# Optimization experiments

Hardware: AMD Instinct MI355X
Metric: run time of the kernel (lower is better)

## Reference

```python
import jax, jax.numpy as jnp
import numpy as np

HEAD_NUM = 16
QKV_DIM = 32
EMB = 512
SQRT_EMB = 22.627416997969522  # sqrt(512)
LOGIT_CLIP = 10.0
BATCH, POMO, PROBLEM = 32, 256, 1024


def setup_inputs() -> dict:
    key = jax.random.key(0)
    ks = jax.random.split(key, 8)
    s = 0.02
    return {
        "encoded_nodes": jax.random.normal(ks[0], (BATCH, PROBLEM, EMB), jnp.float32),
        "encoded_q1": jax.random.normal(ks[1], (BATCH, POMO, EMB), jnp.float32),
        "encoded_last_node": jax.random.normal(ks[2], (BATCH, POMO, EMB), jnp.float32),
        "ninf_mask": jnp.zeros((BATCH, POMO, PROBLEM), jnp.float32),
        # weights stored [in, out] so y = x @ W (equiv. to torch Linear with W.T)
        "Wq_first": jax.random.normal(ks[3], (EMB, HEAD_NUM * QKV_DIM), jnp.float32) * s,
        "Wq_last": jax.random.normal(ks[4], (EMB, HEAD_NUM * QKV_DIM), jnp.float32) * s,
        "Wk": jax.random.normal(ks[5], (EMB, HEAD_NUM * QKV_DIM), jnp.float32) * s,
        "Wv": jax.random.normal(ks[6], (EMB, HEAD_NUM * QKV_DIM), jnp.float32) * s,
        "W_combine": jax.random.normal(ks[7], (HEAD_NUM * QKV_DIM, EMB), jnp.float32) * s,
        "b_combine": jnp.zeros((EMB,), jnp.float32),
    }


def _heads(x):
    # [b, n, h*d] -> [b, h, n, d]
    b, n, _ = x.shape
    return x.reshape(b, n, HEAD_NUM, QKV_DIM).transpose(0, 2, 1, 3)


def reference(encoded_nodes, encoded_q1, encoded_last_node, ninf_mask,
              Wq_first, Wq_last, Wk, Wv, W_combine, b_combine):
    # set_kv
    k = _heads(encoded_nodes @ Wk)                     # [b,h,problem,d]
    v = _heads(encoded_nodes @ Wv)                     # [b,h,problem,d]
    single_head_key = encoded_nodes.transpose(0, 2, 1) # [b,emb,problem]
    # set_q1
    q_first = _heads(encoded_q1 @ Wq_first)            # [b,h,pomo,d]
    # forward
    q_last = _heads(encoded_last_node @ Wq_last)       # [b,h,pomo,d]
    q = q_first + q_last

    scale = 1.0 / jnp.sqrt(jnp.asarray(QKV_DIM, q.dtype))
    score = jnp.einsum("bhnd,bhmd->bhnm", q, k) * scale  # [b,h,pomo,problem]
    score = score + ninf_mask[:, None, :, :]
    weights = jax.nn.softmax(score, axis=-1)
    out = jnp.einsum("bhnm,bhmd->bhnd", weights, v)      # [b,h,pomo,d]
    out_concat = out.transpose(0, 2, 1, 3).reshape(q.shape[0], q.shape[2], HEAD_NUM * QKV_DIM)
    mh_out = out_concat @ W_combine + b_combine          # [b,pomo,emb]

    score2 = jnp.einsum("bne,bem->bnm", mh_out, single_head_key) / SQRT_EMB
    score2 = LOGIT_CLIP * jnp.tanh(score2) + ninf_mask
    probs = jax.nn.softmax(score2, axis=2)               # [b,pomo,problem]
    return probs
```

## Files before the change

### kernel.cpp

```cpp
#include <hip/hip_runtime.h>
#include <math.h>

typedef unsigned short u16;
typedef __attribute__((ext_vector_type(8))) short bf16x8;
typedef __attribute__((ext_vector_type(4))) float f32x4;
typedef __attribute__((ext_vector_type(4))) int i32x4;
typedef __attribute__((ext_vector_type(4))) short s16x4;
typedef __attribute__((ext_vector_type(4))) unsigned short u16x4;

#define MFMA16(a,b,c) __builtin_amdgcn_mfma_f32_16x16x32_bf16((a),(b),(c),0,0,0)

__device__ __forceinline__ u16 f2bf(float x){
  unsigned int u = __float_as_uint(x);
  u += 0x7fffu + ((u >> 16) & 1u);
  return (u16)(u >> 16);
}
__device__ __forceinline__ float bf2f(u16 x){
  return __uint_as_float(((unsigned)x) << 16);
}
__device__ __forceinline__ void gload16(const void* g, void* l){
  __builtin_amdgcn_global_load_lds((const __attribute__((address_space(1))) void*)g,
                                   (__attribute__((address_space(3))) void*)l, 16, 0, 0);
}

__global__ __launch_bounds__(256) void prep(
    const float* __restrict__ nodes, const float* __restrict__ q1, const float* __restrict__ lastn,
    const float* __restrict__ mask,
    const float* __restrict__ Wqf, const float* __restrict__ Wql, const float* __restrict__ Wk,
    const float* __restrict__ Wv, const float* __restrict__ Wc,
    u16* __restrict__ qlbP,
    u16* __restrict__ WtKV, u16* __restrict__ WtQ2, u16* __restrict__ WtCP,
    u16* __restrict__ nodesP, u16* __restrict__ maskP)
{
  const int tid = blockIdx.x * 256 + threadIdx.x;

  #pragma unroll
  for (int it = 0; it < 2; ++it) {
    int id = tid + it*1048576;
    int ln = id & 15, q = (id >> 4) & 3, kc = (id >> 6) & 15, cb = (id >> 10) & 63, b = id >> 16;
    const float* s = nodes + ((b*1024 + cb*16 + ln)*512 + kc*32 + q*8);
    float4 v0 = *(const float4*)s, v1 = *(const float4*)(s+4);
    u16 o[8];
    o[0]=f2bf(v0.x); o[1]=f2bf(v0.y); o[2]=f2bf(v0.z); o[3]=f2bf(v0.w);
    o[4]=f2bf(v1.x); o[5]=f2bf(v1.y); o[6]=f2bf(v1.z); o[7]=f2bf(v1.w);
    *(i32x4*)&nodesP[id*8] = *(i32x4*)&o[0];
  }

  {
    int ln = tid & 15, q = (tid >> 4) & 3, kc = (tid >> 6) & 31, mblk = tid >> 11;
    int m = mblk*16 + ln, k = kc*32 + q*8;
    const float* s = (k < 512) ? (q1 + m*512 + k) : (lastn + m*512 + (k - 512));
    float4 v0 = *(const float4*)s, v1 = *(const float4*)(s+4);
    u16 o[8];
    o[0]=f2bf(v0.x); o[1]=f2bf(v0.y); o[2]=f2bf(v0.z); o[3]=f2bf(v0.w);
    o[4]=f2bf(v1.x); o[5]=f2bf(v1.y); o[6]=f2bf(v1.z); o[7]=f2bf(v1.w);
    *(i32x4*)&qlbP[tid*8] = *(i32x4*)&o[0];
  }

  if (tid < 262144) {
    int n = tid >> 9, k = tid & 511;
    WtQ2[n*1024 + k]       = f2bf(Wqf[k*512 + n]);
    WtQ2[n*1024 + 512 + k] = f2bf(Wql[k*512 + n]);
  }
  if (tid < 524288) {
    int n = tid >> 9, k = tid & 511;
    WtKV[tid] = f2bf(n < 512 ? Wk[k*512 + n] : Wv[k*512 + (n-512)]);
  }
  if (tid < 32768) {
    int ln = tid & 15, q = (tid >> 4) & 3, kc = (tid >> 6) & 15, cb = tid >> 10;
    u16 o[8];
    #pragma unroll
    for (int e=0;e<8;e++) o[e] = f2bf(Wc[(kc*32 + q*8 + e)*512 + cb*16 + ln]);
    *(i32x4*)&WtCP[tid*8] = *(i32x4*)&o[0];
  }
  if (tid < 524288) {
    int brt = tid >> 10, c = tid & 1023;
    const float* mp = mask + (brt*16)*1024 + c;
    u16 vals[16];
    #pragma unroll
    for (int p=0;p<16;p++) vals[p] = f2bf(mp[p*1024]);
    u16* dst = maskP + (brt*64 + (c >> 4))*256 + (c & 15)*4;
    #pragma unroll
    for (int q4=0;q4<4;q4++) {
      u16x4 v; v[0]=vals[q4*4]; v[1]=vals[q4*4+1]; v[2]=vals[q4*4+2]; v[3]=vals[q4*4+3];
      *(u16x4*)&dst[q4*64] = v;
    }
  }
}

__global__ __launch_bounds__(512, 2) void kvq(
    const u16* __restrict__ Akv, const u16* __restrict__ Bkv,
    const u16* __restrict__ Aq,  const u16* __restrict__ Bq,
    u16* __restrict__ Kout, u16* __restrict__ Vout, u16* __restrict__ Qout)
{
  __shared__ u16 smem[24576];
  const int t = threadIdx.x, w = t >> 6, l = t & 63, q = l >> 4, ln = l & 15;
  const int wr = w >> 2, wc = w & 3;
  const int wm = wr * 64, wn = wc * 64;

  const bool isq = blockIdx.x < 128;
  int mb, nb, ksteps, kstr, KC;
  const u16 *Ab, *Bb;
  if (isq) {
    const int bid = blockIdx.x;
    mb = bid >> 1; nb = bid & 1;
    ksteps = 32; kstr = 1024; KC = 32; Ab = Aq; Bb = Bq;
  } else {
    const int bid = blockIdx.x - 128;
    mb = (bid >> 5)*8 + (bid & 7);
    nb = (bid >> 3) & 3;
    ksteps = 16; kstr = 512; KC = 16; Ab = Akv; Bb = Bkv;
  }
  const int m0 = mb*128, n0 = nb*256;

  f32x4 acc[4][4];
  #pragma unroll
  for (int i=0;i<4;i++)
    #pragma unroll
    for (int j=0;j<4;j++)
      #pragma unroll
      for (int r=0;r<4;r++) acc[i][j][r] = 0.f;

  const u16* ApL  = Ab + (((m0 >> 4) + (t >> 6))*KC*64 + (t & 63))*8;
  const u16* Baddr = Bb + (n0 + (t & 255))*kstr + (t >> 8)*8;

  #define STAGE(kc_, b_) { \
    u16* s = smem + (b_)*12288; \
    gload16(ApL + (kc_)*512,       &s[t*8]); \
    gload16(Baddr + (kc_)*32,      &s[4096 + t*8]); \
    gload16(Baddr + 16 + (kc_)*32, &s[4096 + (t+512)*8]); }

  STAGE(0, 0);
  for (int kc = 0; kc < ksteps; kc++) {
    __syncthreads();
    if (kc + 1 < ksteps) STAGE(kc+1, (kc+1)&1);
    const u16* sa = smem + (kc&1)*12288;
    const u16* sb = sa + 4096;
    const int acb = wm >> 4;
    bf16x8 af[4], bfr[4];
    #pragma unroll
    for (int i=0;i<4;i++) af[i]  = *(bf16x8*)&sa[((acb + i)*4 + q)*128 + ln*8];
    #pragma unroll
    for (int j=0;j<4;j++) bfr[j] = *(bf16x8*)&sb[(q*256 + wn + j*16 + ln)*8];
    #pragma unroll
    for (int i=0;i<4;i++)
      #pragma unroll
      for (int j=0;j<4;j++)
        acc[i][j] = MFMA16(af[i], bfr[j], acc[i][j]);
  }
  #undef STAGE

  const float scale = isq ? 0.17677669529663687f : 1.0f;
  const int bb_ = mb >> 3, mloc = (mb & 7)*128;
  const int bbq = mb >> 1, pm0 = (mb & 1)*128;
  for (int h = 0; h < 4; ++h) {
    __syncthreads();
    if (wc == h) {
      #pragma unroll
      for (int i=0;i<4;i++)
        #pragma unroll
        for (int j=0;j<4;j++) {
          s16x4 o;
          #pragma unroll
          for (int r=0;r<4;r++) o[r] = (short)f2bf(acc[i][j][r]*scale);
          *(s16x4*)&smem[(j*16 + ln)*140 + wm + i*16 + q*4] = o;
        }
    }
    __syncthreads();
    #pragma unroll
    for (int hc=0; hc<2; ++hc) {
      if (isq) {
        const int head = nb*8 + h*2 + hc;
        const int m_ = t >> 2, d0 = (t & 3)*8;
        u16 v[8];
        #pragma unroll
        for (int dd=0;dd<8;dd++) v[dd] = smem[(hc*32 + d0 + dd)*140 + m_];
        *(i32x4*)&Qout[((bbq*16 + head)*256 + pm0 + m_)*32 + d0] = *(i32x4*)&v[0];
      } else if (nb < 2) {
        const int head = nb*8 + h*2 + hc;
        const int m_ = t >> 2, d0 = (t & 3)*8;
        u16 v[8];
        #pragma unroll
        for (int dd=0;dd<8;dd++) v[dd] = smem[(hc*32 + d0 + dd)*140 + m_];
        *(i32x4*)&Kout[((bb_*16 + head)*1024 + mloc + m_)*32 + d0] = *(i32x4*)&v[0];
      } else {
        const int vh = (nb-2)*8 + h*2 + hc;
        const int d = t >> 4, mo = (t & 15)*8;
        *(i32x4*)&Vout[((bb_*16 + vh)*32 + d)*1024 + mloc + mo]
            = *(i32x4*)&smem[(hc*32 + d)*140 + mo];
      }
    }
  }
}

__global__ __launch_bounds__(256) void attn(const u16* __restrict__ Qg, const u16* __restrict__ Kg,
                                            const u16* __restrict__ Vtg, const u16* __restrict__ maskP,
                                            u16* __restrict__ Og)
{
  const int bid = blockIdx.x;
  const int bh = (bid & 7)*64 + (bid >> 3);
  const int h = bh & 15, bb = bh >> 4;
  const int t = threadIdx.x, w = t >> 6, l = t & 63, q = l >> 4, ln = l & 15;
  __shared__ u16 Qs[8192];
  __shared__ u16 Ks[4096];
  __shared__ u16 Vs[4096];
  __shared__ u16 Ps[2560];
  u16* Pw = &Ps[w*640];
  const int qbase = (bb*16 + h)*256*32;
  #pragma unroll
  for (int c=0;c<4;c++)
    gload16(&Qg[qbase + t*32 + c*8], &Qs[(c*256 + t)*8]);
  const int kbase = (bb*16 + h)*1024*32;
  const int vbase = (bb*16 + h)*32*1024;
  float rs[4][4];
  f32x4 oacc[4][2];
  #pragma unroll
  for (int rg=0;rg<4;rg++) {
    #pragma unroll
    for (int r=0;r<4;r++) rs[rg][r] = 0.f;
    #pragma unroll
    for (int dt=0;dt<2;dt++)
      #pragma unroll
      for (int r=0;r<4;r++) oacc[rg][dt][r] = 0.f;
  }
  __syncthreads();
  bf16x8 aq[4];
  #pragma unroll
  for (int rg=0;rg<4;rg++) aq[rg] = *(bf16x8*)&Qs[(q*256 + w*64 + rg*16 + ln)*8];
  const u16* mbase = maskP + (bb*16 + w*4)*16384 + q*64 + ln*4;
  u16x4 mqA[8], mqB[8];

  #define RG_BODY(rg, MQC, MQN) { \
    if ((rg) < 3) { \
      _Pragma("unroll") \
      for (int j2=0;j2<8;j2++) \
        MQN[j2] = *(const u16x4*)&mbase[((rg)+1)*16384 + (mc*8 + j2)*256]; \
    } \
    _Pragma("unroll") \
    for (int ch=0; ch<4; ch++) { \
      bf16x8 bk0 = *(bf16x8*)&Ks[(q*128 + (ch*2+0)*16 + ln)*8]; \
      bf16x8 bk1 = *(bf16x8*)&Ks[(q*128 + (ch*2+1)*16 + ln)*8]; \
      f32x4 zz = {0.f,0.f,0.f,0.f}; \
      f32x4 s0 = MFMA16(aq[rg], bk0, zz); \
      f32x4 s1 = MFMA16(aq[rg], bk1, zz); \
      _Pragma("unroll") \
      for (int r=0;r<4;r++) { \
        float e0 = __expf(s0[r] + bf2f(MQC[ch*2+0][r])); \
        float e1 = __expf(s1[r] + bf2f(MQC[ch*2+1][r])); \
        rs[rg][r] += e0 + e1; \
        Pw[(q*4+r)*40 + ln]      = f2bf(e0); \
        Pw[(q*4+r)*40 + 16 + ln] = f2bf(e1); \
      } \
      bf16x8 ap  = *(bf16x8*)&Pw[ln*40 + q*8]; \
      bf16x8 bv0 = *(bf16x8*)&Vs[((ch*4+q)*32 + ln)*8]; \
      bf16x8 bv1 = *(bf16x8*)&Vs[((ch*4+q)*32 + 16 + ln)*8]; \
      oacc[rg][0] = MFMA16(ap, bv0, oacc[rg][0]); \
      oacc[rg][1] = MFMA16(ap, bv1, oacc[rg][1]); \
    } }

  for (int mc = 0; mc < 8; mc++) {
    __syncthreads();
    gload16(&Kg[kbase + (mc*128 + (t & 127))*32 + (t >> 7)*8],       &Ks[t*8]);
    gload16(&Kg[kbase + (mc*128 + (t & 127))*32 + ((t >> 7)+2)*8],   &Ks[(t+256)*8]);
    gload16(&Vtg[vbase + (t & 31)*1024 + mc*128 + (t >> 5)*8],       &Vs[t*8]);
    gload16(&Vtg[vbase + (t & 31)*1024 + mc*128 + ((t >> 5)+8)*8],   &Vs[(t+256)*8]);
    #pragma unroll
    for (int j2=0;j2<8;j2++)
      mqA[j2] = *(const u16x4*)&mbase[(mc*8 + j2)*256];
    __syncthreads();
    RG_BODY(0, mqA, mqB)
    RG_BODY(1, mqB, mqA)
    RG_BODY(2, mqA, mqB)
    RG_BODY(3, mqB, mqA)
  }
  #undef RG_BODY

  #pragma unroll
  for (int rg=0;rg<4;rg++) {
    #pragma unroll
    for (int r=0;r<4;r++) {
      float v = rs[rg][r];
      v += __shfl_xor(v,1); v += __shfl_xor(v,2); v += __shfl_xor(v,4); v += __shfl_xor(v,8);
      rs[rg][r] = __builtin_amdgcn_rcpf(v);
    }
    const int orow = bb*256 + w*64 + rg*16 + q*4;
    #pragma unroll
    for (int dt=0;dt<2;dt++)
      #pragma unroll
      for (int r=0;r<4;r++)
        Og[(orow + r)*512 + h*32 + dt*16 + ln] = f2bf(oacc[rg][dt][r]*rs[rg][r]);
  }
}

__global__ __launch_bounds__(1024) void cmbfin(const u16* __restrict__ oc, const u16* __restrict__ WtCP,
                                               const float* __restrict__ bias,
                                               const u16* __restrict__ nodesP, const u16* __restrict__ maskP,
                                               float* __restrict__ out)
{
  const int bid = blockIdx.x;
  const int bb = bid & 31, rg = bid >> 5;
  const int t = threadIdx.x, w = t >> 6, l = t & 63, q = l >> 4, ln = l & 15;
  __shared__ u16 As[16384];
  __shared__ u16 Ms[16384];
  __shared__ float rsL[16][32];
  const int abase = (bb*256 + rg*32)*512;
  #pragma unroll
  for (int c=0;c<2;c++) {
    int chunk = t + 1024*c;
    gload16(&oc[abase + (chunk & 31)*512 + (chunk >> 5)*8], &As[chunk*8]);
  }
  __syncthreads();
  f32x4 acc1[2][2];
  #pragma unroll
  for (int i=0;i<2;i++)
    #pragma unroll
    for (int ct=0;ct<2;ct++)
      #pragma unroll
      for (int r=0;r<4;r++) acc1[i][ct][r] = 0.f;
  for (int kc=0;kc<16;kc++) {
    bf16x8 af[2];
    #pragma unroll
    for (int i=0;i<2;i++) af[i] = *(bf16x8*)&As[((kc*4 + q)*32 + i*16 + ln)*8];
    #pragma unroll
    for (int ct=0;ct<2;ct++) {
      bf16x8 bfr = *(const bf16x8*)&WtCP[(((w*2 + ct)*16 + kc)*4 + q)*128 + ln*8];
      #pragma unroll
      for (int i=0;i<2;i++) acc1[i][ct] = MFMA16(af[i], bfr, acc1[i][ct]);
    }
  }
  #pragma unroll
  for (int ct=0;ct<2;ct++) {
    int gn = w*32 + ct*16 + ln;
    float bv = bias[gn];
    #pragma unroll
    for (int i=0;i<2;i++)
      #pragma unroll
      for (int r=0;r<4;r++)
        Ms[(gn >> 3)*256 + (i*16 + q*4 + r)*8 + (gn & 7)] = f2bf(acc1[i][ct][r] + bv);
  }
  __syncthreads();
  float rloc[2][4] = {{0.f,0.f,0.f,0.f},{0.f,0.f,0.f,0.f}};
  const int nbase = bb*524288;
  f32x4 acc[2][4];
  #pragma unroll
  for (int i=0;i<2;i++)
    #pragma unroll
    for (int ct=0;ct<4;ct++)
      #pragma unroll
      for (int r=0;r<4;r++) acc[i][ct][r] = 0.f;
  for (int kc=0;kc<16;kc++) {
    bf16x8 af[2];
    #pragma unroll
    for (int i=0;i<2;i++) af[i] = *(bf16x8*)&Ms[((kc*4 + q)*32 + i*16 + ln)*8];
    #pragma unroll
    for (int ct=0;ct<4;ct++) {
      bf16x8 bfr = *(const bf16x8*)&nodesP[nbase + (((w*4 + ct)*16 + kc)*4 + q)*128 + ln*8];
      #pragma unroll
      for (int i=0;i<2;i++) acc[i][ct] = MFMA16(af[i], bfr, acc[i][ct]);
    }
  }
  const float c2 = 0.08838834764831843f;
  const int prow_base = bb*256 + rg*32;
  #pragma unroll
  for (int i=0;i<2;i++) {
    #pragma unroll
    for (int ct=0;ct<4;ct++) {
      u16x4 mv = *(const u16x4*)&maskP[((bb*16 + rg*2 + i)*64 + w*4 + ct)*256 + q*64 + ln*4];
      #pragma unroll
      for (int r=0;r<4;r++) {
        float x = acc[i][ct][r] * c2;
        x = fminf(fmaxf(x, -30.f), 30.f);
        float e2 = __expf(x);
        float lg = 10.f*(e2 - 1.f)*__builtin_amdgcn_rcpf(e2 + 1.f) + bf2f(mv[r]);
        float e = __expf(lg);
        rloc[i][r] += e;
        acc[i][ct][r] = e;
      }
    }
  }
  #pragma unroll
  for (int i=0;i<2;i++)
    #pragma unroll
    for (int r=0;r<4;r++) {
      float v = rloc[i][r];
      v += __shfl_xor(v,1); v += __shfl_xor(v,2); v += __shfl_xor(v,4); v += __shfl_xor(v,8);
      rloc[i][r] = v;
    }
  if (ln == 0) {
    #pragma unroll
    for (int i=0;i<2;i++)
      #pragma unroll
      for (int r=0;r<4;r++) rsL[w][i*16 + q*4 + r] = rloc[i][r];
  }
  __syncthreads();
  float inv[2][4];
  #pragma unroll
  for (int i=0;i<2;i++)
    #pragma unroll
    for (int r=0;r<4;r++) {
      float tot = 0.f;
      #pragma unroll
      for (int ww=0;ww<16;ww++) tot += rsL[ww][i*16 + q*4 + r];
      inv[i][r] = __builtin_amdgcn_rcpf(tot);
    }
  #pragma unroll
  for (int i=0;i<2;i++)
    #pragma unroll
    for (int ct=0;ct<4;ct++) {
      int col0 = w*64 + ct*16 + ln;
      #pragma unroll
      for (int r=0;r<4;r++)
        out[(prow_base + i*16 + q*4 + r)*1024 + col0] = acc[i][ct][r]*inv[i][r];
    }
}

extern "C" void kernel_launch(void* const* d_in, const int* in_sizes, int n_in,
                              void* d_out, int out_size, void* d_ws, size_t ws_size,
                              hipStream_t stream)
{
  (void)in_sizes; (void)n_in; (void)out_size; (void)ws_size;
  const float* nodes = (const float*)d_in[0];
  const float* q1    = (const float*)d_in[1];
  const float* lastn = (const float*)d_in[2];
  const float* mask  = (const float*)d_in[3];
  const float* Wqf   = (const float*)d_in[4];
  const float* Wql   = (const float*)d_in[5];
  const float* Wk    = (const float*)d_in[6];
  const float* Wv    = (const float*)d_in[7];
  const float* Wc    = (const float*)d_in[8];
  const float* bias  = (const float*)d_in[9];
  float* out = (float*)d_out;

  char* p = (char*)d_ws;
  u16* qlbP   = (u16*)p; p += 16777216;
  u16* WtKV   = (u16*)p; p += 1048576;
  u16* WtQ2   = (u16*)p; p += 1048576;
  u16* WtCP   = (u16*)p; p += 524288;
  u16* nodesP = (u16*)p; p += 33554432;
  u16* maskP  = (u16*)p; p += 16777216;
  u16* Kt     = (u16*)p; p += 33554432;
  u16* Vt     = (u16*)p; p += 33554432;
  u16* Qh     = (u16*)p; p += 8388608;
  u16* oc  = qlbP;

  prep<<<4096, 256, 0, stream>>>(nodes, q1, lastn, mask, Wqf, Wql, Wk, Wv, Wc,
                                 qlbP, WtKV, WtQ2, WtCP, nodesP, maskP);
  kvq<<<1152, 512, 0, stream>>>(nodesP, WtKV, qlbP, WtQ2, Kt, Vt, Qh);
  attn<<<512, 256, 0, stream>>>(Qh, Kt, Vt, maskP, oc);
  cmbfin<<<256, 1024, 0, stream>>>(oc, WtCP, bias, nodesP, maskP, out);
}
```

Measured before the change: 342.1 us.

## Double-buffer K/V tiles and ping-pong P scratch in attention kernel

```diff
diff --git a/kernel.cpp b/kernel.cpp
--- a/kernel.cpp
+++ b/kernel.cpp
@@ -202,16 +202,26 @@
   const int h = bh & 15, bb = bh >> 4;
   const int t = threadIdx.x, w = t >> 6, l = t & 63, q = l >> 4, ln = l & 15;
   __shared__ u16 Qs[8192];
-  __shared__ u16 Ks[4096];
-  __shared__ u16 Vs[4096];
-  __shared__ u16 Ps[2560];
-  u16* Pw = &Ps[w*640];
+  __shared__ u16 Ks[2][4096];
+  __shared__ u16 Vs[2][4096];
+  __shared__ u16 Ps[5120];
+  u16* PwA = &Ps[w*640];
+  u16* PwB = &Ps[2560 + w*640];
   const int qbase = (bb*16 + h)*256*32;
   #pragma unroll
   for (int c=0;c<4;c++)
     gload16(&Qg[qbase + t*32 + c*8], &Qs[(c*256 + t)*8]);
   const int kbase = (bb*16 + h)*1024*32;
   const int vbase = (bb*16 + h)*32*1024;
+
+  #define STAGE_KV(mc_, b_) { \
+    gload16(&Kg[kbase + ((mc_)*128 + (t & 127))*32 + (t >> 7)*8],     &Ks[b_][t*8]); \
+    gload16(&Kg[kbase + ((mc_)*128 + (t & 127))*32 + ((t >> 7)+2)*8], &Ks[b_][(t+256)*8]); \
+    gload16(&Vtg[vbase + (t & 31)*1024 + (mc_)*128 + (t >> 5)*8],     &Vs[b_][t*8]); \
+    gload16(&Vtg[vbase + (t & 31)*1024 + (mc_)*128 + ((t >> 5)+8)*8], &Vs[b_][(t+256)*8]); }
+
+  STAGE_KV(0, 0)
+
   float rs[4][4];
   f32x4 oacc[4][2];
   #pragma unroll
@@ -229,17 +239,18 @@
   for (int rg=0;rg<4;rg++) aq[rg] = *(bf16x8*)&Qs[(q*256 + w*64 + rg*16 + ln)*8];
   const u16* mbase = maskP + (bb*16 + w*4)*16384 + q*64 + ln*4;
   u16x4 mqA[8], mqB[8];
-
-  #define RG_BODY(rg, MQC, MQN) { \
-    if ((rg) < 3) { \
-      _Pragma("unroll") \
-      for (int j2=0;j2<8;j2++) \
-        MQN[j2] = *(const u16x4*)&mbase[((rg)+1)*16384 + (mc*8 + j2)*256]; \
-    } \
+  #pragma unroll
+  for (int j2=0;j2<8;j2++) mqA[j2] = *(const u16x4*)&mbase[j2*256];
+
+  #define RG_BODY(rg, MQC, MQN, PRRG, PRMC) { \
+    _Pragma("unroll") \
+    for (int j2=0;j2<8;j2++) \
+      MQN[j2] = *(const u16x4*)&mbase[(PRRG)*16384 + ((PRMC)*8 + j2)*256]; \
     _Pragma("unroll") \
     for (int ch=0; ch<4; ch++) { \
-      bf16x8 bk0 = *(bf16x8*)&Ks[(q*128 + (ch*2+0)*16 + ln)*8]; \
-      bf16x8 bk1 = *(bf16x8*)&Ks[(q*128 + (ch*2+1)*16 + ln)*8]; \
+      u16* Pc = (ch & 1) ? PwB : PwA; \
+      bf16x8 bk0 = *(bf16x8*)&Kc[(q*128 + (ch*2+0)*16 + ln)*8]; \
+      bf16x8 bk1 = *(bf16x8*)&Kc[(q*128 + (ch*2+1)*16 + ln)*8]; \
       f32x4 zz = {0.f,0.f,0.f,0.f}; \
       f32x4 s0 = MFMA16(aq[rg], bk0, zz); \
       f32x4 s1 = MFMA16(aq[rg], bk1, zz); \
@@ -248,32 +259,28 @@
         float e0 = __expf(s0[r] + bf2f(MQC[ch*2+0][r])); \
         float e1 = __expf(s1[r] + bf2f(MQC[ch*2+1][r])); \
         rs[rg][r] += e0 + e1; \
-        Pw[(q*4+r)*40 + ln]      = f2bf(e0); \
-        Pw[(q*4+r)*40 + 16 + ln] = f2bf(e1); \
+        Pc[(q*4+r)*40 + ln]      = f2bf(e0); \
+        Pc[(q*4+r)*40 + 16 + ln] = f2bf(e1); \
       } \
-      bf16x8 ap  = *(bf16x8*)&Pw[ln*40 + q*8]; \
-      bf16x8 bv0 = *(bf16x8*)&Vs[((ch*4+q)*32 + ln)*8]; \
-      bf16x8 bv1 = *(bf16x8*)&Vs[((ch*4+q)*32 + 16 + ln)*8]; \
+      bf16x8 ap  = *(bf16x8*)&Pc[ln*40 + q*8]; \
+      bf16x8 bv0 = *(bf16x8*)&Vc[((ch*4+q)*32 + ln)*8]; \
+      bf16x8 bv1 = *(bf16x8*)&Vc[((ch*4+q)*32 + 16 + ln)*8]; \
       oacc[rg][0] = MFMA16(ap, bv0, oacc[rg][0]); \
       oacc[rg][1] = MFMA16(ap, bv1, oacc[rg][1]); \
     } }
 
   for (int mc = 0; mc < 8; mc++) {
-    __syncthreads();
-    gload16(&Kg[kbase + (mc*128 + (t & 127))*32 + (t >> 7)*8],       &Ks[t*8]);
-    gload16(&Kg[kbase + (mc*128 + (t & 127))*32 + ((t >> 7)+2)*8],   &Ks[(t+256)*8]);
-    gload16(&Vtg[vbase + (t & 31)*1024 + mc*128 + (t >> 5)*8],       &Vs[t*8]);
-    gload16(&Vtg[vbase + (t & 31)*1024 + mc*128 + ((t >> 5)+8)*8],   &Vs[(t+256)*8]);
-    #pragma unroll
-    for (int j2=0;j2<8;j2++)
-      mqA[j2] = *(const u16x4*)&mbase[(mc*8 + j2)*256];
-    __syncthreads();
-    RG_BODY(0, mqA, mqB)
-    RG_BODY(1, mqB, mqA)
-    RG_BODY(2, mqA, mqB)
-    RG_BODY(3, mqB, mqA)
+    if (mc) __syncthreads();
+    if (mc < 7) STAGE_KV(mc+1, (mc+1)&1)
+    const u16* Kc = Ks[mc&1];
+    const u16* Vc = Vs[mc&1];
+    RG_BODY(0, mqA, mqB, 1, mc)
+    RG_BODY(1, mqB, mqA, 2, mc)
+    RG_BODY(2, mqA, mqB, 3, mc)
+    RG_BODY(3, mqB, mqA, 0, (mc+1))
   }
   #undef RG_BODY
+  #undef STAGE_KV
 
   #pragma unroll
   for (int rg=0;rg<4;rg++) {
@@ -317,6 +324,7 @@
     for (int ct=0;ct<2;ct++)
       #pragma unroll
       for (int r=0;r<4;r++) acc1[i][ct][r] = 0.f;
+  #pragma unroll 4
   for (int kc=0;kc<16;kc++) {
     bf16x8 af[2];
     #pragma unroll
@@ -348,6 +356,7 @@
     for (int ct=0;ct<4;ct++)
       #pragma unroll
       for (int r=0;r<4;r++) acc[i][ct][r] = 0.f;
+  #pragma unroll 2
   for (int kc=0;kc<16;kc++) {
     bf16x8 af[2];
     #pragma unroll
```

Result: no change. 338.5 us (-1.1%).
